# Optimization experiments

Measured on AMD Instinct MI355X. Metric: run time of the kernel, lower is better.

The kernel has to match this reference:

```python
import jax, jax.numpy as jnp
import numpy as np

TEMPERATURE = 0.1
TOP_K = 5


def setup_inputs() -> dict:
    key = jax.random.key(0)
    k1, k2 = jax.random.split(key)
    latent = jax.random.normal(k1, (128, 8, 250, 16), dtype=jnp.float32)
    codebook = jax.random.normal(k2, (1024, 8, 250, 16), dtype=jnp.float32) * 0.5
    usage_count = jnp.zeros((1024,), dtype=jnp.float32)
    return {"latent": latent, "codebook": codebook, "usage_count": usage_count}


def reference(latent, codebook, usage_count):
    # soft_quantize_latent
    B = latent.shape[0]
    C = codebook.shape[0]
    lf = latent.reshape(B, -1).astype(jnp.float32)            # [B, D]
    cf = codebook.reshape(C, -1).astype(jnp.float32)          # [C, D]
    # cdist p=2 via expanded squared norms (single GEMM)
    d2 = (jnp.sum(lf * lf, axis=1, keepdims=True)
          + jnp.sum(cf * cf, axis=1)[None, :]
          - 2.0 * (lf @ cf.T))                                 # [B, C]
    dist = jnp.sqrt(jnp.maximum(d2, 0.0))
    # top-k smallest distances
    neg_top, top_idx = jax.lax.top_k(-dist, TOP_K)             # [B, K]
    top_dist = -neg_top
    weights = jax.nn.softmax(-top_dist / TEMPERATURE, axis=1)  # [B, K]
    # weighted codebook combination (gather K rows per batch element)
    quantized = jnp.einsum('bk,bkd->bd', weights, cf[top_idx]).reshape(latent.shape)
    quantized = quantized.astype(latent.dtype)
    # usage update is no_grad in torch: scatter-add stopped weights
    usage_new = usage_count.at[top_idx.reshape(-1)].add(
        jax.lax.stop_gradient(weights).reshape(-1))
    main_indices = top_idx[:, 0]
    main_distances = top_dist[:, 0]
    return (quantized, main_indices, main_distances, usage_new)
```

## Files before the change

### kernel.cpp

```cpp
#include <hip/hip_runtime.h>
#include <math.h>

#define M_B   128
#define N_C   1024
#define K_D   32000
#define NTILE 64
#define KCHUNK 640
#define KSTEP 64
#define NSTAGE (KCHUNK / KSTEP)
#define LDSK  (KSTEP + 8)
#define TOPK  5
#define TEMP  0.1f

typedef short bf16x8 __attribute__((ext_vector_type(8)));
typedef float f32x4  __attribute__((ext_vector_type(4)));

#define WS_CROSS  0
#define WS_CNORM  131072
#define WS_LNORM  132096
#define WS_TOPI   132224
#define WS_TOPW   132864
#define WS_ZERO_N 132224

__global__ void prep(float* __restrict__ ws, const float* __restrict__ usage_in,
                     float* __restrict__ usage_out) {
  const int i = blockIdx.x * 256 + threadIdx.x;
  if (i < WS_ZERO_N) ws[i] = 0.f;
  if (i < N_C) usage_out[i] = usage_in[i];
}

__device__ inline void cvt8(const float4 p0, const float4 p1, uint4& hi,
                            uint4& lo) {
  const unsigned int u0 = __float_as_uint(p0.x), u1 = __float_as_uint(p0.y);
  const unsigned int u2 = __float_as_uint(p0.z), u3 = __float_as_uint(p0.w);
  const unsigned int u4 = __float_as_uint(p1.x), u5 = __float_as_uint(p1.y);
  const unsigned int u6 = __float_as_uint(p1.z), u7 = __float_as_uint(p1.w);
  hi.x = (u0 >> 16) | (u1 & 0xFFFF0000u);
  hi.y = (u2 >> 16) | (u3 & 0xFFFF0000u);
  hi.z = (u4 >> 16) | (u5 & 0xFFFF0000u);
  hi.w = (u6 >> 16) | (u7 & 0xFFFF0000u);
  const float l0 = p0.x - __uint_as_float(u0 & 0xFFFF0000u);
  const float l1 = p0.y - __uint_as_float(u1 & 0xFFFF0000u);
  const float l2 = p0.z - __uint_as_float(u2 & 0xFFFF0000u);
  const float l3 = p0.w - __uint_as_float(u3 & 0xFFFF0000u);
  const float l4 = p1.x - __uint_as_float(u4 & 0xFFFF0000u);
  const float l5 = p1.y - __uint_as_float(u5 & 0xFFFF0000u);
  const float l6 = p1.z - __uint_as_float(u6 & 0xFFFF0000u);
  const float l7 = p1.w - __uint_as_float(u7 & 0xFFFF0000u);
  lo.x = (__float_as_uint(l0) >> 16) | (__float_as_uint(l1) & 0xFFFF0000u);
  lo.y = (__float_as_uint(l2) >> 16) | (__float_as_uint(l3) & 0xFFFF0000u);
  lo.z = (__float_as_uint(l4) >> 16) | (__float_as_uint(l5) & 0xFFFF0000u);
  lo.w = (__float_as_uint(l6) >> 16) | (__float_as_uint(l7) & 0xFFFF0000u);
}

__global__ __launch_bounds__(256, 3) void gemm_dist(
    const float* __restrict__ latent, const float* __restrict__ codebook,
    float* __restrict__ cross, float* __restrict__ cnorm,
    float* __restrict__ lnorm) {
  __shared__ alignas(16) unsigned short Bh[NTILE][LDSK];
  __shared__ alignas(16) unsigned short Bl[NTILE][LDSK];

  const int tid  = threadIdx.x;
  const int nt   = blockIdx.x;
  const int kc   = blockIdx.y;
  const int wave = tid >> 6;
  const int lane = tid & 63;
  const int lrow = lane & 15;
  const int quad = lane >> 4;

  const int brow = tid >> 2;
  const int bcol = (tid & 3) * 16;

  f32x4 acc[2][4];
#pragma unroll
  for (int mt = 0; mt < 2; ++mt)
#pragma unroll
    for (int n = 0; n < 4; ++n) {
      acc[mt][n][0] = 0.f; acc[mt][n][1] = 0.f;
      acc[mt][n][2] = 0.f; acc[mt][n][3] = 0.f;
    }
  float lsq[2] = {0.f, 0.f};
  float csq = 0.f;

  const int kbase = kc * KCHUNK;
  const float* browp = codebook + (size_t)(nt * NTILE + brow) * K_D;

  for (int s = 0; s < NSTAGE; ++s) {
    const int k0 = kbase + s * KSTEP;
    __syncthreads();
#pragma unroll
    for (int u = 0; u < 2; ++u) {
      const int kk = k0 + bcol + u * 8;
      const float4 p0 = *reinterpret_cast<const float4*>(browp + kk);
      const float4 p1 = *reinterpret_cast<const float4*>(browp + kk + 4);
      uint4 hi, lo;
      cvt8(p0, p1, hi, lo);
      *reinterpret_cast<uint4*>(&Bh[brow][bcol + u * 8]) = hi;
      *reinterpret_cast<uint4*>(&Bl[brow][bcol + u * 8]) = lo;
      csq += p0.x * p0.x + p0.y * p0.y + p0.z * p0.z + p0.w * p0.w +
             p1.x * p1.x + p1.y * p1.y + p1.z * p1.z + p1.w * p1.w;
    }
    bf16x8 ah[2][2], al[2][2];
#pragma unroll
    for (int mt = 0; mt < 2; ++mt) {
      const float* arow =
          latent + (size_t)(wave * 32 + mt * 16 + lrow) * K_D + k0 + quad * 8;
#pragma unroll
      for (int kh = 0; kh < 2; ++kh) {
        const float4 p0 = *reinterpret_cast<const float4*>(arow + kh * 32);
        const float4 p1 = *reinterpret_cast<const float4*>(arow + kh * 32 + 4);
        uint4 hi, lo;
        cvt8(p0, p1, hi, lo);
        ah[mt][kh] = *reinterpret_cast<bf16x8*>(&hi);
        al[mt][kh] = *reinterpret_cast<bf16x8*>(&lo);
        if (nt == 0)
          lsq[mt] += p0.x * p0.x + p0.y * p0.y + p0.z * p0.z + p0.w * p0.w +
                     p1.x * p1.x + p1.y * p1.y + p1.z * p1.z + p1.w * p1.w;
      }
    }
    __syncthreads();
#pragma unroll
    for (int kh = 0; kh < 2; ++kh) {
      const int kf = kh * 32 + quad * 8;
#pragma unroll
      for (int n = 0; n < 4; ++n) {
        const bf16x8 bh =
            *reinterpret_cast<const bf16x8*>(&Bh[n * 16 + lrow][kf]);
        const bf16x8 bl =
            *reinterpret_cast<const bf16x8*>(&Bl[n * 16 + lrow][kf]);
#pragma unroll
        for (int mt = 0; mt < 2; ++mt) {
          acc[mt][n] = __builtin_amdgcn_mfma_f32_16x16x32_bf16(
              ah[mt][kh], bh, acc[mt][n], 0, 0, 0);
          acc[mt][n] = __builtin_amdgcn_mfma_f32_16x16x32_bf16(
              ah[mt][kh], bl, acc[mt][n], 0, 0, 0);
          acc[mt][n] = __builtin_amdgcn_mfma_f32_16x16x32_bf16(
              al[mt][kh], bh, acc[mt][n], 0, 0, 0);
        }
      }
    }
  }

#pragma unroll
  for (int mt = 0; mt < 2; ++mt) {
    const int mrow0 = wave * 32 + mt * 16 + quad * 4;
#pragma unroll
    for (int n = 0; n < 4; ++n) {
      const int col = nt * NTILE + n * 16 + lrow;
#pragma unroll
      for (int r = 0; r < 4; ++r)
        atomicAdd(cross + (size_t)(mrow0 + r) * N_C + col, acc[mt][n][r]);
    }
  }

  csq += __shfl_down(csq, 2, 4);
  csq += __shfl_down(csq, 1, 4);
  if ((tid & 3) == 0) atomicAdd(cnorm + nt * NTILE + brow, csq);
  if (nt == 0) {
#pragma unroll
    for (int mt = 0; mt < 2; ++mt) {
      lsq[mt] += __shfl_down(lsq[mt], 32);
      lsq[mt] += __shfl_down(lsq[mt], 16);
      if (lane < 16) atomicAdd(lnorm + wave * 32 + mt * 16 + lane, lsq[mt]);
    }
  }
}

__global__ __launch_bounds__(256) void finalize(
    const float* __restrict__ cross, const float* __restrict__ cnorm,
    const float* __restrict__ lnorm, float* __restrict__ out_idx,
    float* __restrict__ out_dist, float* __restrict__ out_usage,
    int* __restrict__ topidx, float* __restrict__ topw) {
  const int b = blockIdx.x;
  const int tid = threadIdx.x;
  __shared__ float rv[256];
  __shared__ int ri[256];
  __shared__ float seld[TOPK];
  __shared__ int selj[TOPK];

  float d[4];
  bool used[4];
  const float ln = lnorm[b];
#pragma unroll
  for (int i = 0; i < 4; i++) {
    const int j = i * 256 + tid;
    d[i] = ln + cnorm[j] - 2.f * cross[b * N_C + j];
    used[i] = false;
  }
  for (int it = 0; it < TOPK; ++it) {
    float best = 3.4e38f;
    int bj = N_C;
#pragma unroll
    for (int i = 0; i < 4; i++) {
      const int j = i * 256 + tid;
      if (!used[i] && d[i] < best) { best = d[i]; bj = j; }
    }
    rv[tid] = best;
    ri[tid] = bj;
    __syncthreads();
    for (int off = 128; off > 0; off >>= 1) {
      if (tid < off) {
        const float ov = rv[tid + off];
        const int oj = ri[tid + off];
        if (ov < rv[tid] || (ov == rv[tid] && oj < ri[tid])) {
          rv[tid] = ov;
          ri[tid] = oj;
        }
      }
      __syncthreads();
    }
    const int jw = ri[0];
    const float dw = rv[0];
    if (tid == 0) { selj[it] = jw; seld[it] = dw; }
    if ((jw & 255) == tid) used[jw >> 8] = true;
    __syncthreads();
  }
  if (tid == 0) {
    float dist[TOPK], w[TOPK], wsum = 0.f;
#pragma unroll
    for (int k = 0; k < TOPK; k++) dist[k] = sqrtf(fmaxf(seld[k], 0.f));
#pragma unroll
    for (int k = 0; k < TOPK; k++) {
      w[k] = expf((dist[0] - dist[k]) / TEMP);
      wsum += w[k];
    }
#pragma unroll
    for (int k = 0; k < TOPK; k++) {
      w[k] /= wsum;
      topidx[b * TOPK + k] = selj[k];
      topw[b * TOPK + k] = w[k];
      atomicAdd(out_usage + selj[k], w[k]);
    }
    out_idx[b] = (float)selj[0];
    out_dist[b] = dist[0];
  }
}

__global__ __launch_bounds__(256) void quantize(
    const float* __restrict__ codebook, const int* __restrict__ topidx,
    const float* __restrict__ topw, float* __restrict__ out) {
  const int b = blockIdx.y;
  const int dc = blockIdx.x;
  const int tid = threadIdx.x;
  int idx[TOPK];
  float w[TOPK];
#pragma unroll
  for (int k = 0; k < TOPK; k++) {
    idx[k] = topidx[b * TOPK + k];
    w[k] = topw[b * TOPK + k];
  }
  const int f4base = dc * 1000;
#pragma unroll
  for (int s = 0; s < 4; s++) {
    const int f = tid + s * 256;
    if (f < 1000) {
      const int dpos = (f4base + f) * 4;
      float4 q = {0.f, 0.f, 0.f, 0.f};
#pragma unroll
      for (int k = 0; k < TOPK; k++) {
        const float4 c = *reinterpret_cast<const float4*>(
            codebook + (size_t)idx[k] * K_D + dpos);
        q.x += w[k] * c.x;
        q.y += w[k] * c.y;
        q.z += w[k] * c.z;
        q.w += w[k] * c.w;
      }
      *reinterpret_cast<float4*>(out + (size_t)b * K_D + dpos) = q;
    }
  }
}

extern "C" void kernel_launch(void* const* d_in, const int* in_sizes, int n_in,
                              void* d_out, int out_size, void* d_ws,
                              size_t ws_size, hipStream_t stream) {
  const float* latent = (const float*)d_in[0];
  const float* codebook = (const float*)d_in[1];
  const float* usage_in = (const float*)d_in[2];

  float* out = (float*)d_out;
  float* quant = out;
  float* out_idx = out + 4096000;
  float* out_dist = out + 4096128;
  float* out_usage = out + 4096256;

  float* ws = (float*)d_ws;
  float* cross = ws + WS_CROSS;
  float* cnorm = ws + WS_CNORM;
  float* lnorm = ws + WS_LNORM;
  int* topidx = (int*)(ws + WS_TOPI);
  float* topw = ws + WS_TOPW;

  prep<<<(WS_ZERO_N + 255) / 256, 256, 0, stream>>>(ws, usage_in, out_usage);
  gemm_dist<<<dim3(16, 50), 256, 0, stream>>>(latent, codebook, cross, cnorm,
                                              lnorm);
  finalize<<<128, 256, 0, stream>>>(cross, cnorm, lnorm, out_idx, out_dist,
                                    out_usage, topidx, topw);
  quantize<<<dim3(8, 128), 256, 0, stream>>>(codebook, topidx, topw, quant);
}
```

Before: 266.6 us.

## Double-buffer codebook LDS tiles and halve K-chunk to raise occupancy

Adds a two-stage LDS double buffer for the codebook tile, so the next stage's global loads are issued before the barrier and written into the alternate buffer after the MFMA work. This removes one __syncthreads per stage. The latent loads are also issued up front. KCHUNK is halved, which doubles the grid to 1600 blocks, and launch bounds rise to 4 blocks per CU for more parallelism. In exchange, LDS use doubles, register pressure rises from the prefetched values, and atomicAdd traffic on the cross and norm buffers doubles.

```diff
diff --git a/kernel.cpp b/kernel.cpp
--- a/kernel.cpp
+++ b/kernel.cpp
@@ -5,7 +5,7 @@
 #define N_C   1024
 #define K_D   32000
 #define NTILE 64
-#define KCHUNK 640
+#define KCHUNK 320
 #define KSTEP 64
 #define NSTAGE (KCHUNK / KSTEP)
 #define LDSK  (KSTEP + 8)
@@ -53,12 +53,17 @@
   lo.w = (__float_as_uint(l6) >> 16) | (__float_as_uint(l7) & 0xFFFF0000u);
 }
 
-__global__ __launch_bounds__(256, 3) void gemm_dist(
+__device__ inline float sq8(const float4 p0, const float4 p1) {
+  return p0.x * p0.x + p0.y * p0.y + p0.z * p0.z + p0.w * p0.w +
+         p1.x * p1.x + p1.y * p1.y + p1.z * p1.z + p1.w * p1.w;
+}
+
+__global__ __launch_bounds__(256, 4) void gemm_dist(
     const float* __restrict__ latent, const float* __restrict__ codebook,
     float* __restrict__ cross, float* __restrict__ cnorm,
     float* __restrict__ lnorm) {
-  __shared__ alignas(16) unsigned short Bh[NTILE][LDSK];
-  __shared__ alignas(16) unsigned short Bl[NTILE][LDSK];
+  __shared__ alignas(16) unsigned short Bh[2][NTILE][LDSK];
+  __shared__ alignas(16) unsigned short Bl[2][NTILE][LDSK];
 
   const int tid  = threadIdx.x;
   const int nt   = blockIdx.x;
@@ -85,60 +90,83 @@
   const int kbase = kc * KCHUNK;
   const float* browp = codebook + (size_t)(nt * NTILE + brow) * K_D;
 
+#pragma unroll
+  for (int u = 0; u < 2; ++u) {
+    const int kk = kbase + bcol + u * 8;
+    const float4 p0 = *reinterpret_cast<const float4*>(browp + kk);
+    const float4 p1 = *reinterpret_cast<const float4*>(browp + kk + 4);
+    uint4 hi, lo;
+    cvt8(p0, p1, hi, lo);
+    *reinterpret_cast<uint4*>(&Bh[0][brow][bcol + u * 8]) = hi;
+    *reinterpret_cast<uint4*>(&Bl[0][brow][bcol + u * 8]) = lo;
+    csq += sq8(p0, p1);
+  }
+
+  int cur = 0;
   for (int s = 0; s < NSTAGE; ++s) {
     const int k0 = kbase + s * KSTEP;
+    float4 ap[2][2][2];
+#pragma unroll
+    for (int kh = 0; kh < 2; ++kh)
+#pragma unroll
+      for (int mt = 0; mt < 2; ++mt) {
+        const float* ar = latent +
+                          (size_t)(wave * 32 + mt * 16 + lrow) * K_D + k0 +
+                          kh * 32 + quad * 8;
+        ap[kh][mt][0] = *reinterpret_cast<const float4*>(ar);
+        ap[kh][mt][1] = *reinterpret_cast<const float4*>(ar + 4);
+      }
+    float4 bp[2][2];
+    if (s + 1 < NSTAGE) {
+      const int kn = kbase + (s + 1) * KSTEP + bcol;
+#pragma unroll
+      for (int u = 0; u < 2; ++u) {
+        bp[u][0] = *reinterpret_cast<const float4*>(browp + kn + u * 8);
+        bp[u][1] = *reinterpret_cast<const float4*>(browp + kn + u * 8 + 4);
+      }
+    }
     __syncthreads();
 #pragma unroll
-    for (int u = 0; u < 2; ++u) {
-      const int kk = k0 + bcol + u * 8;
-      const float4 p0 = *reinterpret_cast<const float4*>(browp + kk);
-      const float4 p1 = *reinterpret_cast<const float4*>(browp + kk + 4);
-      uint4 hi, lo;
-      cvt8(p0, p1, hi, lo);
-      *reinterpret_cast<uint4*>(&Bh[brow][bcol + u * 8]) = hi;
-      *reinterpret_cast<uint4*>(&Bl[brow][bcol + u * 8]) = lo;
-      csq += p0.x * p0.x + p0.y * p0.y + p0.z * p0.z + p0.w * p0.w +
-             p1.x * p1.x + p1.y * p1.y + p1.z * p1.z + p1.w * p1.w;
-    }
-    bf16x8 ah[2][2], al[2][2];
-#pragma unroll
-    for (int mt = 0; mt < 2; ++mt) {
-      const float* arow =
-          latent + (size_t)(wave * 32 + mt * 16 + lrow) * K_D + k0 + quad * 8;
-#pragma unroll
-      for (int kh = 0; kh < 2; ++kh) {
-        const float4 p0 = *reinterpret_cast<const float4*>(arow + kh * 32);
-        const float4 p1 = *reinterpret_cast<const float4*>(arow + kh * 32 + 4);
+    for (int kh = 0; kh < 2; ++kh) {
+      bf16x8 ah[2], al[2];
+#pragma unroll
+      for (int mt = 0; mt < 2; ++mt) {
         uint4 hi, lo;
-        cvt8(p0, p1, hi, lo);
-        ah[mt][kh] = *reinterpret_cast<bf16x8*>(&hi);
-        al[mt][kh] = *reinterpret_cast<bf16x8*>(&lo);
-        if (nt == 0)
-          lsq[mt] += p0.x * p0.x + p0.y * p0.y + p0.z * p0.z + p0.w * p0.w +
-                     p1.x * p1.x + p1.y * p1.y + p1.z * p1.z + p1.w * p1.w;
-      }
-    }
-    __syncthreads();
-#pragma unroll
-    for (int kh = 0; kh < 2; ++kh) {
+        cvt8(ap[kh][mt][0], ap[kh][mt][1], hi, lo);
+        ah[mt] = *reinterpret_cast<bf16x8*>(&hi);
+        al[mt] = *reinterpret_cast<bf16x8*>(&lo);
+        if (nt == 0) lsq[mt] += sq8(ap[kh][mt][0], ap[kh][mt][1]);
+      }
       const int kf = kh * 32 + quad * 8;
 #pragma unroll
       for (int n = 0; n < 4; ++n) {
         const bf16x8 bh =
-            *reinterpret_cast<const bf16x8*>(&Bh[n * 16 + lrow][kf]);
+            *reinterpret_cast<const bf16x8*>(&Bh[cur][n * 16 + lrow][kf]);
         const bf16x8 bl =
-            *reinterpret_cast<const bf16x8*>(&Bl[n * 16 + lrow][kf]);
+            *reinterpret_cast<const bf16x8*>(&Bl[cur][n * 16 + lrow][kf]);
 #pragma unroll
         for (int mt = 0; mt < 2; ++mt) {
           acc[mt][n] = __builtin_amdgcn_mfma_f32_16x16x32_bf16(
-              ah[mt][kh], bh, acc[mt][n], 0, 0, 0);
+              ah[mt], bh, acc[mt][n], 0, 0, 0);
           acc[mt][n] = __builtin_amdgcn_mfma_f32_16x16x32_bf16(
-              ah[mt][kh], bl, acc[mt][n], 0, 0, 0);
+              ah[mt], bl, acc[mt][n], 0, 0, 0);
           acc[mt][n] = __builtin_amdgcn_mfma_f32_16x16x32_bf16(
-              al[mt][kh], bh, acc[mt][n], 0, 0, 0);
+              al[mt], bh, acc[mt][n], 0, 0, 0);
         }
       }
     }
+    if (s + 1 < NSTAGE) {
+      const int nxt = cur ^ 1;
+#pragma unroll
+      for (int u = 0; u < 2; ++u) {
+        uint4 hi, lo;
+        cvt8(bp[u][0], bp[u][1], hi, lo);
+        *reinterpret_cast<uint4*>(&Bh[nxt][brow][bcol + u * 8]) = hi;
+        *reinterpret_cast<uint4*>(&Bl[nxt][brow][bcol + u * 8]) = lo;
+        csq += sq8(bp[u][0], bp[u][1]);
+      }
+    }
+    cur ^= 1;
   }
 
 #pragma unroll
@@ -291,8 +319,8 @@
   float* topw = ws + WS_TOPW;
 
   prep<<<(WS_ZERO_N + 255) / 256, 256, 0, stream>>>(ws, usage_in, out_usage);
-  gemm_dist<<<dim3(16, 50), 256, 0, stream>>>(latent, codebook, cross, cnorm,
-                                              lnorm);
+  gemm_dist<<<dim3(16, 100), 256, 0, stream>>>(latent, codebook, cross, cnorm,
+                                               lnorm);
   finalize<<<128, 256, 0, stream>>>(cross, cnorm, lnorm, out_idx, out_dist,
                                     out_usage, topidx, topw);
   quantize<<<dim3(8, 128), 256, 0, stream>>>(codebook, topidx, topw, quant);
```

New measurement: 256.5 us. 1.04x faster.

## Double-buffer GEMM stages, replace atomics with split-K partials, drop prep kernel

Applied to the files above, without the earlier changes.

Restructures the split-K distance GEMM. Tiles shrink to 32 codebook rows and grow to 1280-wide K chunks, and the LDS B tile is double-buffered with register prefetch of the next latent and codebook slices. Atomic accumulation into a zeroed workspace is replaced by plain per-chunk partial stores (with codebook norm folded in) written into the quantized output buffer, and finalize sums them. The latent norm moves into finalize and the prep kernel is removed, with the usage copy folded into one GEMM block. This removes the atomics and one launch, but finalize now does strided reads over 25 partials per element plus a full latent row read.

```diff
diff --git a/kernel.cpp b/kernel.cpp
--- a/kernel.cpp
+++ b/kernel.cpp
@@ -4,8 +4,10 @@
 #define M_B   128
 #define N_C   1024
 #define K_D   32000
-#define NTILE 64
-#define KCHUNK 640
+#define NTILE 32
+#define NNT   (N_C / NTILE)
+#define KCHUNK 1280
+#define NKC   (K_D / KCHUNK)
 #define KSTEP 64
 #define NSTAGE (KCHUNK / KSTEP)
 #define LDSK  (KSTEP + 8)
@@ -15,19 +17,15 @@
 typedef short bf16x8 __attribute__((ext_vector_type(8)));
 typedef float f32x4  __attribute__((ext_vector_type(4)));
 
-#define WS_CROSS  0
-#define WS_CNORM  131072
-#define WS_LNORM  132096
-#define WS_TOPI   132224
-#define WS_TOPW   132864
-#define WS_ZERO_N 132224
-
-__global__ void prep(float* __restrict__ ws, const float* __restrict__ usage_in,
-                     float* __restrict__ usage_out) {
-  const int i = blockIdx.x * 256 + threadIdx.x;
-  if (i < WS_ZERO_N) ws[i] = 0.f;
-  if (i < N_C) usage_out[i] = usage_in[i];
-}
+#define WS_TOPI 0
+#define WS_TOPW 640
+
+#define LDS_BARRIER()                                        \
+  do {                                                       \
+    asm volatile("s_waitcnt lgkmcnt(0)" ::: "memory");       \
+    __builtin_amdgcn_s_barrier();                            \
+    __builtin_amdgcn_sched_barrier(0);                       \
+  } while (0)
 
 __device__ inline void cvt8(const float4 p0, const float4 p1, uint4& hi,
                             uint4& lo) {
@@ -53,124 +51,170 @@
   lo.w = (__float_as_uint(l6) >> 16) | (__float_as_uint(l7) & 0xFFFF0000u);
 }
 
-__global__ __launch_bounds__(256, 3) void gemm_dist(
+__device__ inline float sq8(const float4 p0, const float4 p1) {
+  return p0.x * p0.x + p0.y * p0.y + p0.z * p0.z + p0.w * p0.w +
+         p1.x * p1.x + p1.y * p1.y + p1.z * p1.z + p1.w * p1.w;
+}
+
+__global__ __launch_bounds__(256, 4) void gemm_dist(
     const float* __restrict__ latent, const float* __restrict__ codebook,
-    float* __restrict__ cross, float* __restrict__ cnorm,
-    float* __restrict__ lnorm) {
-  __shared__ alignas(16) unsigned short Bh[NTILE][LDSK];
-  __shared__ alignas(16) unsigned short Bl[NTILE][LDSK];
-
-  const int tid  = threadIdx.x;
-  const int nt   = blockIdx.x;
-  const int kc   = blockIdx.y;
+    const float* __restrict__ usage_in, float* __restrict__ usage_out,
+    float* __restrict__ partial) {
+  __shared__ alignas(16) unsigned short Bh[2][NTILE][LDSK];
+  __shared__ alignas(16) unsigned short Bl[2][NTILE][LDSK];
+  __shared__ float cnl[NTILE];
+
+  const int tid = threadIdx.x;
+  const int nt  = blockIdx.x;
+  const int kc  = blockIdx.y;
+
+  if (nt == 0 && kc == 0) {
+#pragma unroll
+    for (int j = 0; j < 4; ++j)
+      usage_out[tid + j * 256] = usage_in[tid + j * 256];
+  }
+
   const int wave = tid >> 6;
   const int lane = tid & 63;
   const int lrow = lane & 15;
   const int quad = lane >> 4;
 
-  const int brow = tid >> 2;
-  const int bcol = (tid & 3) * 16;
-
-  f32x4 acc[2][4];
+  const int brow = tid >> 3;
+  const int bcol = (tid & 7) * 8;
+
+  f32x4 acc[2][2];
 #pragma unroll
   for (int mt = 0; mt < 2; ++mt)
 #pragma unroll
-    for (int n = 0; n < 4; ++n) {
+    for (int n = 0; n < 2; ++n) {
       acc[mt][n][0] = 0.f; acc[mt][n][1] = 0.f;
       acc[mt][n][2] = 0.f; acc[mt][n][3] = 0.f;
     }
-  float lsq[2] = {0.f, 0.f};
   float csq = 0.f;
 
   const int kbase = kc * KCHUNK;
   const float* browp = codebook + (size_t)(nt * NTILE + brow) * K_D;
 
-  for (int s = 0; s < NSTAGE; ++s) {
-    const int k0 = kbase + s * KSTEP;
-    __syncthreads();
-#pragma unroll
-    for (int u = 0; u < 2; ++u) {
-      const int kk = k0 + bcol + u * 8;
-      const float4 p0 = *reinterpret_cast<const float4*>(browp + kk);
-      const float4 p1 = *reinterpret_cast<const float4*>(browp + kk + 4);
-      uint4 hi, lo;
-      cvt8(p0, p1, hi, lo);
-      *reinterpret_cast<uint4*>(&Bh[brow][bcol + u * 8]) = hi;
-      *reinterpret_cast<uint4*>(&Bl[brow][bcol + u * 8]) = lo;
-      csq += p0.x * p0.x + p0.y * p0.y + p0.z * p0.z + p0.w * p0.w +
-             p1.x * p1.x + p1.y * p1.y + p1.z * p1.z + p1.w * p1.w;
-    }
-    bf16x8 ah[2][2], al[2][2];
-#pragma unroll
-    for (int mt = 0; mt < 2; ++mt) {
-      const float* arow =
-          latent + (size_t)(wave * 32 + mt * 16 + lrow) * K_D + k0 + quad * 8;
-#pragma unroll
-      for (int kh = 0; kh < 2; ++kh) {
-        const float4 p0 = *reinterpret_cast<const float4*>(arow + kh * 32);
-        const float4 p1 = *reinterpret_cast<const float4*>(arow + kh * 32 + 4);
-        uint4 hi, lo;
-        cvt8(p0, p1, hi, lo);
-        ah[mt][kh] = *reinterpret_cast<bf16x8*>(&hi);
-        al[mt][kh] = *reinterpret_cast<bf16x8*>(&lo);
-        if (nt == 0)
-          lsq[mt] += p0.x * p0.x + p0.y * p0.y + p0.z * p0.z + p0.w * p0.w +
-                     p1.x * p1.x + p1.y * p1.y + p1.z * p1.z + p1.w * p1.w;
-      }
-    }
-    __syncthreads();
+  {
+    const float4 p0 = *reinterpret_cast<const float4*>(browp + kbase + bcol);
+    const float4 p1 =
+        *reinterpret_cast<const float4*>(browp + kbase + bcol + 4);
+    uint4 hi, lo;
+    cvt8(p0, p1, hi, lo);
+    *reinterpret_cast<uint4*>(&Bh[0][brow][bcol]) = hi;
+    *reinterpret_cast<uint4*>(&Bl[0][brow][bcol]) = lo;
+    csq += sq8(p0, p1);
+  }
+  float4 ap[2][2][2];
+#pragma unroll
+  for (int mt = 0; mt < 2; ++mt) {
+    const float* arow =
+        latent + (size_t)(wave * 32 + mt * 16 + lrow) * K_D + kbase + quad * 8;
 #pragma unroll
     for (int kh = 0; kh < 2; ++kh) {
-      const int kf = kh * 32 + quad * 8;
-#pragma unroll
-      for (int n = 0; n < 4; ++n) {
-        const bf16x8 bh =
-            *reinterpret_cast<const bf16x8*>(&Bh[n * 16 + lrow][kf]);
-        const bf16x8 bl =
-            *reinterpret_cast<const bf16x8*>(&Bl[n * 16 + lrow][kf]);
-#pragma unroll
-        for (int mt = 0; mt < 2; ++mt) {
-          acc[mt][n] = __builtin_amdgcn_mfma_f32_16x16x32_bf16(
-              ah[mt][kh], bh, acc[mt][n], 0, 0, 0);
-          acc[mt][n] = __builtin_amdgcn_mfma_f32_16x16x32_bf16(
-              ah[mt][kh], bl, acc[mt][n], 0, 0, 0);
-          acc[mt][n] = __builtin_amdgcn_mfma_f32_16x16x32_bf16(
-              al[mt][kh], bh, acc[mt][n], 0, 0, 0);
-        }
-      }
-    }
-  }
-
+      ap[mt][kh][0] = *reinterpret_cast<const float4*>(arow + kh * 32);
+      ap[mt][kh][1] = *reinterpret_cast<const float4*>(arow + kh * 32 + 4);
+    }
+  }
+  float4 bpA[2], bpB[2];
+  bpA[0] = *reinterpret_cast<const float4*>(browp + kbase + KSTEP + bcol);
+  bpA[1] = *reinterpret_cast<const float4*>(browp + kbase + KSTEP + bcol + 4);
+  LDS_BARRIER();
+
+#define HALF_STEP(P, S, BCUR, BNXT)                                           \
+  {                                                                           \
+                    \
+    bf16x8 ah[2][2], al[2][2];                                                \
+    _Pragma("unroll") for (int mt = 0; mt < 2; ++mt) {                        \
+      _Pragma("unroll") for (int kh = 0; kh < 2; ++kh) {                      \
+        uint4 hi, lo;                                                         \
+        cvt8(ap[mt][kh][0], ap[mt][kh][1], hi, lo);                           \
+        ah[mt][kh] = *reinterpret_cast<bf16x8*>(&hi);                         \
+        al[mt][kh] = *reinterpret_cast<bf16x8*>(&lo);                         \
+      }                                                                       \
+    }                                                                         \
+     \
+    {                                                                         \
+      const int ks = kbase + ((S) + 1 < NSTAGE ? (S) + 1 : (S)) * KSTEP;      \
+      _Pragma("unroll") for (int mt = 0; mt < 2; ++mt) {                      \
+        const float* arow = latent +                                          \
+            (size_t)(wave * 32 + mt * 16 + lrow) * K_D + ks + quad * 8;       \
+        _Pragma("unroll") for (int kh = 0; kh < 2; ++kh) {                    \
+          ap[mt][kh][0] = *reinterpret_cast<const float4*>(arow + kh * 32);   \
+          ap[mt][kh][1] =                                                     \
+              *reinterpret_cast<const float4*>(arow + kh * 32 + 4);           \
+        }                                                                     \
+      }                                                                       \
+    }                                                                         \
+                                                       \
+    _Pragma("unroll") for (int kh = 0; kh < 2; ++kh) {                        \
+      const int kf = kh * 32 + quad * 8;                                      \
+      _Pragma("unroll") for (int n = 0; n < 2; ++n) {                         \
+        const bf16x8 bh =                                                     \
+            *reinterpret_cast<const bf16x8*>(&Bh[P][n * 16 + lrow][kf]);      \
+        const bf16x8 bl =                                                     \
+            *reinterpret_cast<const bf16x8*>(&Bl[P][n * 16 + lrow][kf]);      \
+        _Pragma("unroll") for (int mt = 0; mt < 2; ++mt) {                    \
+          acc[mt][n] = __builtin_amdgcn_mfma_f32_16x16x32_bf16(               \
+              ah[mt][kh], bh, acc[mt][n], 0, 0, 0);                           \
+          acc[mt][n] = __builtin_amdgcn_mfma_f32_16x16x32_bf16(               \
+              ah[mt][kh], bl, acc[mt][n], 0, 0, 0);                           \
+          acc[mt][n] = __builtin_amdgcn_mfma_f32_16x16x32_bf16(               \
+              al[mt][kh], bh, acc[mt][n], 0, 0, 0);                           \
+        }                                                                     \
+      }                                                                       \
+    }                                                                         \
+            \
+    if ((S) + 1 < NSTAGE) {                                                   \
+      uint4 hi, lo;                                                           \
+      cvt8(BCUR[0], BCUR[1], hi, lo);                                         \
+      *reinterpret_cast<uint4*>(&Bh[(P) ^ 1][brow][bcol]) = hi;               \
+      *reinterpret_cast<uint4*>(&Bl[(P) ^ 1][brow][bcol]) = lo;               \
+      csq += sq8(BCUR[0], BCUR[1]);                                           \
+    }                                                                         \
+           \
+    {                                                                         \
+      const int kn =                                                          \
+          kbase + ((S) + 2 < NSTAGE ? (S) + 2 : NSTAGE - 1) * KSTEP + bcol;   \
+      BNXT[0] = *reinterpret_cast<const float4*>(browp + kn);                 \
+      BNXT[1] = *reinterpret_cast<const float4*>(browp + kn + 4);             \
+    }                                                                         \
+    LDS_BARRIER();                                                            \
+  }
+
+  for (int it = 0; it < NSTAGE / 2; ++it) {
+    const int s0 = it * 2;
+    HALF_STEP(0, s0, bpA, bpB)
+    HALF_STEP(1, s0 + 1, bpB, bpA)
+  }
+#undef HALF_STEP
+
+  csq += __shfl_down(csq, 4, 8);
+  csq += __shfl_down(csq, 2, 8);
+  csq += __shfl_down(csq, 1, 8);
+  if ((tid & 7) == 0) cnl[brow] = csq;
+  __syncthreads();
+
+  float* pbase = partial + (size_t)(kc * NNT + nt) * (M_B * NTILE);
 #pragma unroll
   for (int mt = 0; mt < 2; ++mt) {
-    const int mrow0 = wave * 32 + mt * 16 + quad * 4;
-#pragma unroll
-    for (int n = 0; n < 4; ++n) {
-      const int col = nt * NTILE + n * 16 + lrow;
+    const int r0 = wave * 32 + mt * 16 + quad * 4;
+#pragma unroll
+    for (int n = 0; n < 2; ++n) {
+      const int col = n * 16 + lrow;
+      const float cn = cnl[col];
 #pragma unroll
       for (int r = 0; r < 4; ++r)
-        atomicAdd(cross + (size_t)(mrow0 + r) * N_C + col, acc[mt][n][r]);
-    }
-  }
-
-  csq += __shfl_down(csq, 2, 4);
-  csq += __shfl_down(csq, 1, 4);
-  if ((tid & 3) == 0) atomicAdd(cnorm + nt * NTILE + brow, csq);
-  if (nt == 0) {
-#pragma unroll
-    for (int mt = 0; mt < 2; ++mt) {
-      lsq[mt] += __shfl_down(lsq[mt], 32);
-      lsq[mt] += __shfl_down(lsq[mt], 16);
-      if (lane < 16) atomicAdd(lnorm + wave * 32 + mt * 16 + lane, lsq[mt]);
+        pbase[(r0 + r) * NTILE + col] = cn - 2.f * acc[mt][n][r];
     }
   }
 }
 
 __global__ __launch_bounds__(256) void finalize(
-    const float* __restrict__ cross, const float* __restrict__ cnorm,
-    const float* __restrict__ lnorm, float* __restrict__ out_idx,
-    float* __restrict__ out_dist, float* __restrict__ out_usage,
-    int* __restrict__ topidx, float* __restrict__ topw) {
+    const float* __restrict__ latent, const float* __restrict__ partial,
+    float* __restrict__ out_idx, float* __restrict__ out_dist,
+    float* __restrict__ out_usage, int* __restrict__ topidx,
+    float* __restrict__ topw) {
   const int b = blockIdx.x;
   const int tid = threadIdx.x;
   __shared__ float rv[256];
@@ -178,13 +222,32 @@
   __shared__ float seld[TOPK];
   __shared__ int selj[TOPK];
 
+  float lsq = 0.f;
+  const float4* lrow4 =
+      reinterpret_cast<const float4*>(latent + (size_t)b * K_D);
+  for (int f = tid; f < K_D / 4; f += 256) {
+    const float4 p = lrow4[f];
+    lsq += p.x * p.x + p.y * p.y + p.z * p.z + p.w * p.w;
+  }
+  rv[tid] = lsq;
+  __syncthreads();
+  for (int off = 128; off > 0; off >>= 1) {
+    if (tid < off) rv[tid] += rv[tid + off];
+    __syncthreads();
+  }
+  const float ln = rv[0];
+  __syncthreads();
+
   float d[4];
   bool used[4];
-  const float ln = lnorm[b];
 #pragma unroll
   for (int i = 0; i < 4; i++) {
     const int j = i * 256 + tid;
-    d[i] = ln + cnorm[j] - 2.f * cross[b * N_C + j];
+    float s = ln;
+    const size_t off0 = (size_t)(j >> 5) * (M_B * NTILE) + b * NTILE + (j & 31);
+    for (int kc = 0; kc < NKC; ++kc)
+      s += partial[off0 + (size_t)kc * NNT * (M_B * NTILE)];
+    d[i] = s;
     used[i] = false;
   }
   for (int it = 0; it < TOPK; ++it) {
@@ -284,16 +347,14 @@
   float* out_usage = out + 4096256;
 
   float* ws = (float*)d_ws;
-  float* cross = ws + WS_CROSS;
-  float* cnorm = ws + WS_CNORM;
-  float* lnorm = ws + WS_LNORM;
   int* topidx = (int*)(ws + WS_TOPI);
   float* topw = ws + WS_TOPW;
 
-  prep<<<(WS_ZERO_N + 255) / 256, 256, 0, stream>>>(ws, usage_in, out_usage);
-  gemm_dist<<<dim3(16, 50), 256, 0, stream>>>(latent, codebook, cross, cnorm,
-                                              lnorm);
-  finalize<<<128, 256, 0, stream>>>(cross, cnorm, lnorm, out_idx, out_dist,
+  float* partial = quant;
+
+  gemm_dist<<<dim3(NNT, NKC), 256, 0, stream>>>(latent, codebook, usage_in,
+                                                out_usage, partial);
+  finalize<<<128, 256, 0, stream>>>(latent, partial, out_idx, out_dist,
                                     out_usage, topidx, topw);
   quantize<<<dim3(8, 128), 256, 0, stream>>>(codebook, topidx, topw, quant);
 }
```

After: 298.7 us. 12.0% more time.

## Pipeline codebook tiles via async global-to-LDS loads with 4-deep buffering

Applied to the files above, without the earlier changes.

Replaces the synchronous codebook load, convert and LDS store with direct global_load_lds transfers of raw fp32 into a 4-slot swizzled LDS ring, prefetching three stages ahead. The bf16 hi/lo split now happens after reading from LDS, and the latent operands are register-prefetched one stage ahead. This aims to hide global memory latency and drop one barrier per stage. In exchange it uses more LDS, lowers the occupancy target from 3 to 2 blocks, repeats the conversion work per wave, and moves the codebook norm computation onto wave 0.

```diff
diff --git a/kernel.cpp b/kernel.cpp
--- a/kernel.cpp
+++ b/kernel.cpp
@@ -8,26 +8,31 @@
 #define KCHUNK 640
 #define KSTEP 64
 #define NSTAGE (KCHUNK / KSTEP)
-#define LDSK  (KSTEP + 8)
+#define NBUF  4
 #define TOPK  5
 #define TEMP  0.1f
 
 typedef short bf16x8 __attribute__((ext_vector_type(8)));
 typedef float f32x4  __attribute__((ext_vector_type(4)));
 
-#define WS_CROSS  0
-#define WS_CNORM  131072
-#define WS_LNORM  132096
-#define WS_TOPI   132224
-#define WS_TOPW   132864
-#define WS_ZERO_N 132224
-
-__global__ void prep(float* __restrict__ ws, const float* __restrict__ usage_in,
-                     float* __restrict__ usage_out) {
-  const int i = blockIdx.x * 256 + threadIdx.x;
-  if (i < WS_ZERO_N) ws[i] = 0.f;
-  if (i < N_C) usage_out[i] = usage_in[i];
-}
+#define WS_CROSS   0
+#define WS_CNORM   131072
+#define WS_LNORM   132096
+#define WS_TOPI    132224
+#define WS_TOPW    132864
+#define WS_ZERO_N  132224
+
+#define GLOAD16(g, l)                                            \
+  __builtin_amdgcn_global_load_lds(                              \
+      (const __attribute__((address_space(1))) void*)(g),        \
+      (__attribute__((address_space(3))) void*)(l), 16, 0, 0)
+
+#define LDS_BARRIER()                                        \
+  do {                                                       \
+    asm volatile("s_waitcnt lgkmcnt(0)" ::: "memory");       \
+    __builtin_amdgcn_s_barrier();                            \
+    __builtin_amdgcn_sched_barrier(0);                       \
+  } while (0)
 
 __device__ inline void cvt8(const float4 p0, const float4 p1, uint4& hi,
                             uint4& lo) {
@@ -53,12 +58,23 @@
   lo.w = (__float_as_uint(l6) >> 16) | (__float_as_uint(l7) & 0xFFFF0000u);
 }
 
-__global__ __launch_bounds__(256, 3) void gemm_dist(
+__device__ inline float sq8(const float4 p0, const float4 p1) {
+  return p0.x * p0.x + p0.y * p0.y + p0.z * p0.z + p0.w * p0.w +
+         p1.x * p1.x + p1.y * p1.y + p1.z * p1.z + p1.w * p1.w;
+}
+
+__global__ void prep(float* __restrict__ ws, const float* __restrict__ usage_in,
+                     float* __restrict__ usage_out) {
+  const int i = blockIdx.x * 256 + threadIdx.x;
+  if (i < WS_ZERO_N) ws[i] = 0.f;
+  if (i < N_C) usage_out[i] = usage_in[i];
+}
+
+__global__ __launch_bounds__(256, 2) void gemm_dist(
     const float* __restrict__ latent, const float* __restrict__ codebook,
     float* __restrict__ cross, float* __restrict__ cnorm,
     float* __restrict__ lnorm) {
-  __shared__ alignas(16) unsigned short Bh[NTILE][LDSK];
-  __shared__ alignas(16) unsigned short Bl[NTILE][LDSK];
+  __shared__ float buf[NBUF][NTILE * KSTEP];
 
   const int tid  = threadIdx.x;
   const int nt   = blockIdx.x;
@@ -67,9 +83,17 @@
   const int lane = tid & 63;
   const int lrow = lane & 15;
   const int quad = lane >> 4;
-
-  const int brow = tid >> 2;
-  const int bcol = (tid & 3) * 16;
+  const int kbase = kc * KCHUNK;
+
+  size_t gofs[4];
+  int lofs[4];
+#pragma unroll
+  for (int i = 0; i < 4; ++i) {
+    const int row = wave * 16 + i * 4 + (lane >> 4);
+    gofs[i] =
+        (size_t)(nt * NTILE + row) * K_D + (((lane & 15) ^ (row & 7)) << 2);
+    lofs[i] = wave * 1024 + i * 256 + lane * 4;
+  }
 
   f32x4 acc[2][4];
 #pragma unroll
@@ -79,55 +103,76 @@
       acc[mt][n][0] = 0.f; acc[mt][n][1] = 0.f;
       acc[mt][n][2] = 0.f; acc[mt][n][3] = 0.f;
     }
+  float csqn[4] = {0.f, 0.f, 0.f, 0.f};
   float lsq[2] = {0.f, 0.f};
-  float csq = 0.f;
-
-  const int kbase = kc * KCHUNK;
-  const float* browp = codebook + (size_t)(nt * NTILE + brow) * K_D;
-
+
+  const size_t arow0 = (size_t)(wave * 32 + lrow) * K_D + quad * 8;
+  float4 ap[2][2][2];
+
+#pragma unroll
+  for (int mt = 0; mt < 2; ++mt) {
+    const float* ar = latent + arow0 + (size_t)mt * 16 * K_D + kbase;
+#pragma unroll
+    for (int kh = 0; kh < 2; ++kh) {
+      ap[mt][kh][0] = *reinterpret_cast<const float4*>(ar + kh * 32);
+      ap[mt][kh][1] = *reinterpret_cast<const float4*>(ar + kh * 32 + 4);
+    }
+  }
+#pragma unroll
+  for (int b = 0; b < 3; ++b)
+#pragma unroll
+    for (int i = 0; i < 4; ++i)
+      GLOAD16(codebook + gofs[i] + kbase + b * KSTEP, &buf[b][lofs[i]]);
+  asm volatile("s_waitcnt vmcnt(8)" ::: "memory");
+  __builtin_amdgcn_s_barrier();
+  __builtin_amdgcn_sched_barrier(0);
+
+#pragma unroll
   for (int s = 0; s < NSTAGE; ++s) {
-    const int k0 = kbase + s * KSTEP;
-    __syncthreads();
-#pragma unroll
-    for (int u = 0; u < 2; ++u) {
-      const int kk = k0 + bcol + u * 8;
-      const float4 p0 = *reinterpret_cast<const float4*>(browp + kk);
-      const float4 p1 = *reinterpret_cast<const float4*>(browp + kk + 4);
-      uint4 hi, lo;
-      cvt8(p0, p1, hi, lo);
-      *reinterpret_cast<uint4*>(&Bh[brow][bcol + u * 8]) = hi;
-      *reinterpret_cast<uint4*>(&Bl[brow][bcol + u * 8]) = lo;
-      csq += p0.x * p0.x + p0.y * p0.y + p0.z * p0.z + p0.w * p0.w +
-             p1.x * p1.x + p1.y * p1.y + p1.z * p1.z + p1.w * p1.w;
-    }
+    const float* bufr = buf[s & 3];
     bf16x8 ah[2][2], al[2][2];
 #pragma unroll
-    for (int mt = 0; mt < 2; ++mt) {
-      const float* arow =
-          latent + (size_t)(wave * 32 + mt * 16 + lrow) * K_D + k0 + quad * 8;
+    for (int mt = 0; mt < 2; ++mt)
 #pragma unroll
       for (int kh = 0; kh < 2; ++kh) {
-        const float4 p0 = *reinterpret_cast<const float4*>(arow + kh * 32);
-        const float4 p1 = *reinterpret_cast<const float4*>(arow + kh * 32 + 4);
         uint4 hi, lo;
-        cvt8(p0, p1, hi, lo);
+        cvt8(ap[mt][kh][0], ap[mt][kh][1], hi, lo);
         ah[mt][kh] = *reinterpret_cast<bf16x8*>(&hi);
         al[mt][kh] = *reinterpret_cast<bf16x8*>(&lo);
-        if (nt == 0)
-          lsq[mt] += p0.x * p0.x + p0.y * p0.y + p0.z * p0.z + p0.w * p0.w +
-                     p1.x * p1.x + p1.y * p1.y + p1.z * p1.z + p1.w * p1.w;
-      }
-    }
-    __syncthreads();
+        if (nt == 0) lsq[mt] += sq8(ap[mt][kh][0], ap[mt][kh][1]);
+      }
+    if (s + 1 < NSTAGE) {
+#pragma unroll
+      for (int mt = 0; mt < 2; ++mt) {
+        const float* ar = latent + arow0 + (size_t)mt * 16 * K_D + kbase +
+                          (s + 1) * KSTEP;
+#pragma unroll
+        for (int kh = 0; kh < 2; ++kh) {
+          ap[mt][kh][0] = *reinterpret_cast<const float4*>(ar + kh * 32);
+          ap[mt][kh][1] = *reinterpret_cast<const float4*>(ar + kh * 32 + 4);
+        }
+      }
+    }
+    if (s + 3 < NSTAGE) {
+#pragma unroll
+      for (int i = 0; i < 4; ++i)
+        GLOAD16(codebook + gofs[i] + kbase + (s + 3) * KSTEP,
+                &buf[(s + 3) & 3][lofs[i]]);
+    }
 #pragma unroll
     for (int kh = 0; kh < 2; ++kh) {
-      const int kf = kh * 32 + quad * 8;
 #pragma unroll
       for (int n = 0; n < 4; ++n) {
-        const bf16x8 bh =
-            *reinterpret_cast<const bf16x8*>(&Bh[n * 16 + lrow][kf]);
-        const bf16x8 bl =
-            *reinterpret_cast<const bf16x8*>(&Bl[n * 16 + lrow][kf]);
+        const int row = n * 16 + lrow;
+        const int fb = row * 64 + kh * 32 +
+                       ((quad ^ ((row >> 1) & 3)) << 3) + ((row & 1) << 2);
+        const float4 f0 = *reinterpret_cast<const float4*>(&bufr[fb]);
+        const float4 f1 = *reinterpret_cast<const float4*>(&bufr[fb ^ 4]);
+        uint4 hi, lo;
+        cvt8(f0, f1, hi, lo);
+        const bf16x8 bh = *reinterpret_cast<bf16x8*>(&hi);
+        const bf16x8 bl = *reinterpret_cast<bf16x8*>(&lo);
+        if (wave == 0) csqn[n] += sq8(f0, f1);
 #pragma unroll
         for (int mt = 0; mt < 2; ++mt) {
           acc[mt][n] = __builtin_amdgcn_mfma_f32_16x16x32_bf16(
@@ -139,6 +184,7 @@
         }
       }
     }
+    if (s + 1 < NSTAGE) LDS_BARRIER();
   }
 
 #pragma unroll
@@ -152,16 +198,22 @@
         atomicAdd(cross + (size_t)(mrow0 + r) * N_C + col, acc[mt][n][r]);
     }
   }
-
-  csq += __shfl_down(csq, 2, 4);
-  csq += __shfl_down(csq, 1, 4);
-  if ((tid & 3) == 0) atomicAdd(cnorm + nt * NTILE + brow, csq);
+  if (wave == 0) {
+#pragma unroll
+    for (int n = 0; n < 4; ++n) {
+      float c = csqn[n];
+      c += __shfl_down(c, 32);
+      c += __shfl_down(c, 16);
+      if (lane < 16) atomicAdd(cnorm + nt * NTILE + n * 16 + lane, c);
+    }
+  }
   if (nt == 0) {
 #pragma unroll
     for (int mt = 0; mt < 2; ++mt) {
-      lsq[mt] += __shfl_down(lsq[mt], 32);
-      lsq[mt] += __shfl_down(lsq[mt], 16);
-      if (lane < 16) atomicAdd(lnorm + wave * 32 + mt * 16 + lane, lsq[mt]);
+      float v = lsq[mt];
+      v += __shfl_down(v, 32);
+      v += __shfl_down(v, 16);
+      if (lane < 16) atomicAdd(lnorm + wave * 32 + mt * 16 + lane, v);
     }
   }
 }
```

After: 268.7 us. About the same (+0.8%).
